# Kernel optimization log

Hardware: AMD Instinct MI355X
Metric: run time of the kernel (lower is better)

## Reference

```python
import jax, jax.numpy as jnp
import numpy as np

V = 20000
E = 40000
NODE_IN = 74
EDGE_IN = 12
D = 64            # node_out_feats
EH = 128          # edge_hidden_feats
STEPS = 6         # num_step_message_passing


def setup_inputs() -> dict:
    key = jax.random.key(0)
    ks = jax.random.split(key, 16)
    s = lambda k, shape, scale=0.05: jax.random.normal(k, shape, dtype=jnp.float32) * scale
    return {
        "node_feats": jax.random.normal(ks[0], (V, NODE_IN), dtype=jnp.float32),
        "edge_feats": jax.random.normal(ks[1], (E, EDGE_IN), dtype=jnp.float32),
        "src": jax.random.randint(ks[2], (E,), 0, V),
        "dst": jax.random.randint(ks[3], (E,), 0, V),
        # project_node_feats: Linear(NODE_IN, D) + ReLU
        "proj_W": s(ks[4], (D, NODE_IN)),
        "proj_b": jnp.zeros((D,), jnp.float32),
        # NNConv edge network: Linear(EDGE_IN, EH) -> ReLU -> Linear(EH, D*D)
        "en_W1": s(ks[5], (EH, EDGE_IN)),
        "en_b1": jnp.zeros((EH,), jnp.float32),
        "en_W2": s(ks[6], (D * D, EH)),
        "en_b2": jnp.zeros((D * D,), jnp.float32),
        # NNConv output bias
        "conv_b": jnp.zeros((D,), jnp.float32),
        # single-layer GRU (PyTorch gate order r, z, n)
        "gru_Wih": s(ks[7], (3 * D, D)),
        "gru_Whh": s(ks[8], (3 * D, D)),
        "gru_bih": jnp.zeros((3 * D,), jnp.float32),
        "gru_bhh": jnp.zeros((3 * D,), jnp.float32),
        # MLPPredictor: Linear(2*D, 1)
        "pred_W": s(ks[9], (1, 2 * D)),
        "pred_b": jnp.zeros((1,), jnp.float32),
    }


def reference(node_feats, edge_feats, src, dst, proj_W, proj_b,
              en_W1, en_b1, en_W2, en_b2, conv_b,
              gru_Wih, gru_Whh, gru_bih, gru_bhh, pred_W, pred_b):
    nV = node_feats.shape[0]
    # project node features
    h = jax.nn.relu(node_feats @ proj_W.T + proj_b)  # (V, D)
    # per-edge weight matrices from the edge network (constant across steps)
    ew = jax.nn.relu(edge_feats @ en_W1.T + en_b1) @ en_W2.T + en_b2  # (E, D*D)
    ew = ew.reshape(-1, D, D)  # (E, D, D)

    def step(h, _):
        # NNConv (aggregator='sum'): m_e = h[src_e] @ W_e, sum at dst, + bias
        m = jnp.einsum('ei,eio->eo', h[src], ew)               # (E, D)
        neigh = jax.ops.segment_sum(m, dst, num_segments=nV)   # (V, D)
        x = jax.nn.relu(neigh + conv_b)
        # GRU update; hidden == h (they coincide in the original loop)
        gi = x @ gru_Wih.T + gru_bih
        gh = h @ gru_Whh.T + gru_bhh
        i_r, i_z, i_n = jnp.split(gi, 3, axis=-1)
        h_r, h_z, h_n = jnp.split(gh, 3, axis=-1)
        r = jax.nn.sigmoid(i_r + h_r)
        z = jax.nn.sigmoid(i_z + h_z)
        n = jnp.tanh(i_n + r * h_n)
        h_new = (1.0 - z) * n + z * h
        return h_new, None

    h, _ = jax.lax.scan(step, h, None, length=STEPS)
    # MLPPredictor: per-edge gather-concat-linear
    score = jnp.concatenate([h[src], h[dst]], axis=1) @ pred_W.T + pred_b  # (E, 1)
    return score
```

## Files before the change

### kernel.cpp

```cpp
#include <hip/hip_runtime.h>
#include <hip/hip_bf16.h>
#include <cstdint>

#define NV 20000
#define NE 40000
#define NODE_IN 74
#define EDGE_IN 12
#define D 64
#define EHID 128
#define NSTEPS 6

typedef __bf16 bf16x8 __attribute__((ext_vector_type(8)));
typedef float f32x4 __attribute__((ext_vector_type(4)));

__global__ __launch_bounds__(256) void k_proj(const float* __restrict__ nf,
                                              const float* __restrict__ W,
                                              const float* __restrict__ b,
                                              float* __restrict__ h,
                                              float* __restrict__ neigh) {
  __shared__ float sn[4][NODE_IN];
  int tid = threadIdx.x;
  int nb = blockIdx.x * 4;
  for (int idx = tid; idx < 4 * NODE_IN; idx += 256) {
    int r = idx / NODE_IN, c = idx % NODE_IN;
    sn[r][c] = nf[(size_t)(nb + r) * NODE_IN + c];
  }
  __syncthreads();
  int nl = tid >> 6, o = tid & 63;
  float acc = b[o];
#pragma unroll
  for (int i = 0; i < NODE_IN; ++i) acc = fmaf(sn[nl][i], W[o * NODE_IN + i], acc);
  h[(size_t)(nb + nl) * D + o] = fmaxf(acc, 0.f);
  neigh[(size_t)(nb + nl) * D + o] = 0.f;
}

__global__ __launch_bounds__(256) void k_edge1(const float* __restrict__ ef,
                                               const float* __restrict__ W1,
                                               const float* __restrict__ b1,
                                               __hip_bfloat16* __restrict__ t_bf) {
  __shared__ float se[2][EDGE_IN];
  int tid = threadIdx.x;
  int eb = blockIdx.x * 2;
  if (tid < 2 * EDGE_IN)
    se[tid / EDGE_IN][tid % EDGE_IN] =
        ef[(size_t)(eb + tid / EDGE_IN) * EDGE_IN + tid % EDGE_IN];
  __syncthreads();
  int el = tid >> 7, k = tid & 127;
  float acc = b1[k];
#pragma unroll
  for (int j = 0; j < EDGE_IN; ++j) acc = fmaf(se[el][j], W1[k * EDGE_IN + j], acc);
  t_bf[(size_t)(eb + el) * EHID + k] = __float2bfloat16(fmaxf(acc, 0.f));
}

__global__ __launch_bounds__(256) void k_cvt_w2(const float* __restrict__ W2,
                                                __hip_bfloat16* __restrict__ w2b) {
  int idx = blockIdx.x * 256 + threadIdx.x;
  if (idx < D * D * EHID) w2b[idx] = __float2bfloat16(W2[idx]);
}

__global__ __launch_bounds__(256) void k_b2t(const float* __restrict__ b2,
                                             __hip_bfloat16* __restrict__ b2t) {
  int idx = blockIdx.x * 256 + threadIdx.x;
  int o = idx >> 6, i = idx & 63;
  b2t[o * 64 + i] = __float2bfloat16(b2[i * 64 + o]);
}

__global__ __launch_bounds__(256) void k_build_b(const float* __restrict__ Wih,
                                                 const float* __restrict__ Whh,
                                                 __hip_bfloat16* __restrict__ Bhi,
                                                 __hip_bfloat16* __restrict__ Blo) {
  int idx = blockIdx.x * 256 + threadIdx.x;
  int n = idx >> 7, k = idx & 127;
  int o = n & 63, cls = n >> 6;
  float v;
  if (cls == 0)      v = (k < 64) ? Wih[o * 64 + k]         : Whh[o * 64 + (k - 64)];
  else if (cls == 1) v = (k < 64) ? Wih[(64 + o) * 64 + k]  : Whh[(64 + o) * 64 + (k - 64)];
  else if (cls == 2) v = (k < 64) ? Wih[(128 + o) * 64 + k] : 0.f;
  else               v = (k < 64) ? 0.f                     : Whh[(128 + o) * 64 + (k - 64)];
  __hip_bfloat16 hi = __float2bfloat16(v);
  Bhi[idx] = hi;
  Blo[idx] = __float2bfloat16(v - __bfloat162float(hi));
}

__global__ __launch_bounds__(512, 2) void k_msg(const float* __restrict__ h,
                                                const __hip_bfloat16* __restrict__ t_bf,
                                                const __hip_bfloat16* __restrict__ w2,
                                                const __hip_bfloat16* __restrict__ b2t,
                                                const int* __restrict__ src,
                                                const int* __restrict__ dst,
                                                float* __restrict__ neigh) {
  __shared__ __hip_bfloat16 W2s[512 * 128];
  __shared__ __hip_bfloat16 Hs[4][32 * 64];
  int tid = threadIdx.x;
  int bx = blockIdx.x;
  int cg = bx >> 6, ih = (bx >> 5) & 1, s = bx & 31;
  int lane = tid & 63, lr = lane & 15, lq = lane >> 4;
  int wave = tid >> 6;
  int team = wave >> 1, mthalf = wave & 1;
  int lane128 = tid & 127;
  const int ocol = cg * 16 + lr;

#pragma unroll
  for (int it = 0; it < 16; ++it) {
    int chunk = it * 512 + tid;
    int row = chunk >> 4, c = chunk & 15;
    int ig = row >> 4, ol = row & 15;
    const __hip_bfloat16* gp =
        w2 + ((size_t)((ih * 32 + ig) * 64 + cg * 16 + ol)) * EHID + c * 8;
    *(bf16x8*)(W2s + row * 128 + ((c ^ ol) * 8)) = *(const bf16x8*)gp;
  }
  bf16x8 b2frag = *(const bf16x8*)(b2t + (size_t)ocol * 64 + ih * 32 + lq * 8);

  int nt = (s < 31) ? 20 : 5;

#pragma unroll 1
  for (int r5 = 0; r5 < 5; ++r5) {
    int t = r5 * 4 + team;
    int e0t = s * 1280 + t * 64;
    bool valid = (t < nt);
    __syncthreads();
    if (valid) {
      int e_l = lane128 & 63, hh = lane128 >> 6;
      int s_e = src[e0t + e_l];
      const float* hrow = h + (size_t)s_e * D + ih * 32 + hh * 16;
#pragma unroll
      for (int j4 = 0; j4 < 4; ++j4) {
        float4 hv = *(const float4*)(hrow + j4 * 4);
        int i0 = hh * 16 + j4 * 4;
        Hs[team][(i0 + 0) * 64 + e_l] = __float2bfloat16(hv.x);
        Hs[team][(i0 + 1) * 64 + e_l] = __float2bfloat16(hv.y);
        Hs[team][(i0 + 2) * 64 + e_l] = __float2bfloat16(hv.z);
        Hs[team][(i0 + 3) * 64 + e_l] = __float2bfloat16(hv.w);
      }
    }
    __syncthreads();
    if (!valid) continue;

    const __hip_bfloat16* Ht = Hs[team];
    int mt2 = mthalf * 2;
    bf16x8 tf[2][4];
#pragma unroll
    for (int mt = 0; mt < 2; ++mt)
#pragma unroll
      for (int ks = 0; ks < 4; ++ks)
        tf[mt][ks] = *(const bf16x8*)(t_bf + (size_t)(e0t + (mt2 + mt) * 16 + lr) * EHID +
                                      ks * 32 + lq * 8);
    f32x4 C0, C1;
    {
      bf16x8 af0, af1;
#pragma unroll
      for (int j = 0; j < 8; ++j) {
        af0[j] = *(const __bf16*)(Ht + (lq * 8 + j) * 64 + mt2 * 16 + lr);
        af1[j] = *(const __bf16*)(Ht + (lq * 8 + j) * 64 + (mt2 + 1) * 16 + lr);
      }
      f32x4 z = {0.f, 0.f, 0.f, 0.f};
      C0 = __builtin_amdgcn_mfma_f32_16x16x32_bf16(af0, b2frag, z, 0, 0, 0);
      C1 = __builtin_amdgcn_mfma_f32_16x16x32_bf16(af1, b2frag, z, 0, 0, 0);
    }
    int sw0 = (((0 * 4 + lq) ^ lr) * 8);
    int sw1 = (((1 * 4 + lq) ^ lr) * 8);
    int sw2 = (((2 * 4 + lq) ^ lr) * 8);
    int sw3 = (((3 * 4 + lq) ^ lr) * 8);
    int e0q0 = mt2 * 16 + lq * 4;
    int e0q1 = (mt2 + 1) * 16 + lq * 4;

#pragma unroll 2
    for (int ig = 0; ig < 32; ++ig) {
      const __hip_bfloat16* Wr = W2s + (ig * 16 + lr) * 128;
      bf16x8 f0 = *(const bf16x8*)(Wr + sw0);
      bf16x8 f1 = *(const bf16x8*)(Wr + sw1);
      bf16x8 f2 = *(const bf16x8*)(Wr + sw2);
      bf16x8 f3 = *(const bf16x8*)(Wr + sw3);
      uint2 hA = *(const uint2*)(Ht + ig * 64 + e0q0);
      uint2 hB = *(const uint2*)(Ht + ig * 64 + e0q1);
      f32x4 P0 = {0.f, 0.f, 0.f, 0.f};
      P0 = __builtin_amdgcn_mfma_f32_16x16x32_bf16(tf[0][0], f0, P0, 0, 0, 0);
      P0 = __builtin_amdgcn_mfma_f32_16x16x32_bf16(tf[0][1], f1, P0, 0, 0, 0);
      P0 = __builtin_amdgcn_mfma_f32_16x16x32_bf16(tf[0][2], f2, P0, 0, 0, 0);
      P0 = __builtin_amdgcn_mfma_f32_16x16x32_bf16(tf[0][3], f3, P0, 0, 0, 0);
      f32x4 P1 = {0.f, 0.f, 0.f, 0.f};
      P1 = __builtin_amdgcn_mfma_f32_16x16x32_bf16(tf[1][0], f0, P1, 0, 0, 0);
      P1 = __builtin_amdgcn_mfma_f32_16x16x32_bf16(tf[1][1], f1, P1, 0, 0, 0);
      P1 = __builtin_amdgcn_mfma_f32_16x16x32_bf16(tf[1][2], f2, P1, 0, 0, 0);
      P1 = __builtin_amdgcn_mfma_f32_16x16x32_bf16(tf[1][3], f3, P1, 0, 0, 0);
      C0[0] = fmaf(__uint_as_float(hA.x << 16), P0[0], C0[0]);
      C0[1] = fmaf(__uint_as_float(hA.x & 0xffff0000u), P0[1], C0[1]);
      C0[2] = fmaf(__uint_as_float(hA.y << 16), P0[2], C0[2]);
      C0[3] = fmaf(__uint_as_float(hA.y & 0xffff0000u), P0[3], C0[3]);
      C1[0] = fmaf(__uint_as_float(hB.x << 16), P1[0], C1[0]);
      C1[1] = fmaf(__uint_as_float(hB.x & 0xffff0000u), P1[1], C1[1]);
      C1[2] = fmaf(__uint_as_float(hB.y << 16), P1[2], C1[2]);
      C1[3] = fmaf(__uint_as_float(hB.y & 0xffff0000u), P1[3], C1[3]);
    }
#pragma unroll
    for (int r = 0; r < 4; ++r) {
      int ea = e0t + e0q0 + r;
      atomicAdd(neigh + (size_t)dst[ea] * D + ocol, C0[r]);
      int eb = e0t + e0q1 + r;
      atomicAdd(neigh + (size_t)dst[eb] * D + ocol, C1[r]);
    }
  }
}

__global__ __launch_bounds__(256) void k_gru(float* __restrict__ neigh,
                                             float* __restrict__ h,
                                             const __hip_bfloat16* __restrict__ Bhi,
                                             const __hip_bfloat16* __restrict__ Blo,
                                             const float* __restrict__ cb,
                                             const float* __restrict__ bih,
                                             const float* __restrict__ bhh) {
  __shared__ __hip_bfloat16 Ahi[64 * 128];
  __shared__ __hip_bfloat16 Alo[64 * 128];
  int tid = threadIdx.x;
  int n0 = blockIdx.x * 64;
  for (int idx = tid; idx < 64 * 64; idx += 256) {
    int node = idx >> 6, f = idx & 63;
    int gn = n0 + node;
    int gc = gn < NV ? gn : NV - 1;
    float xv = fmaxf(neigh[(size_t)gc * D + f] + cb[f], 0.f);
    if (gn < NV) neigh[(size_t)gn * D + f] = 0.f;
    float hv = h[(size_t)gc * D + f];
    __hip_bfloat16 xh = __float2bfloat16(xv);
    __hip_bfloat16 hh = __float2bfloat16(hv);
    Ahi[node * 128 + f] = xh;
    Ahi[node * 128 + 64 + f] = hh;
    Alo[node * 128 + f] = __float2bfloat16(xv - __bfloat162float(xh));
    Alo[node * 128 + 64 + f] = __float2bfloat16(hv - __bfloat162float(hh));
  }
  __syncthreads();
  int wave = tid >> 6, lane = tid & 63;
  int lr = lane & 15, lq = lane >> 4;
  f32x4 acc[4][4] = {};
#pragma unroll
  for (int ks = 0; ks < 4; ++ks) {
    int koff = ks * 32 + lq * 8;
    bf16x8 ah[4], al[4], bh[4], bl[4];
#pragma unroll
    for (int mt = 0; mt < 4; ++mt) {
      ah[mt] = *(const bf16x8*)(Ahi + (mt * 16 + lr) * 128 + koff);
      al[mt] = *(const bf16x8*)(Alo + (mt * 16 + lr) * 128 + koff);
    }
#pragma unroll
    for (int cls = 0; cls < 4; ++cls) {
      int n = cls * 64 + wave * 16 + lr;
      bh[cls] = *(const bf16x8*)(Bhi + (size_t)n * 128 + koff);
      bl[cls] = *(const bf16x8*)(Blo + (size_t)n * 128 + koff);
    }
#pragma unroll
    for (int mt = 0; mt < 4; ++mt)
#pragma unroll
      for (int cls = 0; cls < 4; ++cls) {
        acc[mt][cls] = __builtin_amdgcn_mfma_f32_16x16x32_bf16(ah[mt], bh[cls], acc[mt][cls], 0, 0, 0);
        acc[mt][cls] = __builtin_amdgcn_mfma_f32_16x16x32_bf16(al[mt], bh[cls], acc[mt][cls], 0, 0, 0);
        acc[mt][cls] = __builtin_amdgcn_mfma_f32_16x16x32_bf16(ah[mt], bl[cls], acc[mt][cls], 0, 0, 0);
      }
  }
  int o = wave * 16 + lr;
  float b_r = bih[o] + bhh[o];
  float b_z = bih[64 + o] + bhh[64 + o];
  float b_in = bih[128 + o];
  float b_hn = bhh[128 + o];
#pragma unroll
  for (int mt = 0; mt < 4; ++mt) {
#pragma unroll
    for (int r = 0; r < 4; ++r) {
      int gn = n0 + mt * 16 + lq * 4 + r;
      if (gn < NV) {
        float rs = acc[mt][0][r] + b_r;
        float zs = acc[mt][1][r] + b_z;
        float inn = acc[mt][2][r] + b_in;
        float hnn = acc[mt][3][r] + b_hn;
        float rg = 1.f / (1.f + __expf(-rs));
        float zg = 1.f / (1.f + __expf(-zs));
        float a = inn + rg * hnn;
        a = fminf(fmaxf(a, -15.f), 15.f);
        float e2 = __expf(2.f * a);
        float nn = (e2 - 1.f) / (e2 + 1.f);
        float hold = h[(size_t)gn * D + o];
        h[(size_t)gn * D + o] = (1.f - zg) * nn + zg * hold;
      }
    }
  }
}

__global__ __launch_bounds__(256) void k_pred(const float* __restrict__ h,
                                              const int* __restrict__ src,
                                              const int* __restrict__ dst,
                                              const float* __restrict__ pW,
                                              const float* __restrict__ pb,
                                              float* __restrict__ out) {
  int wave = threadIdx.x >> 6, lane = threadIdx.x & 63;
  int e = blockIdx.x * 4 + wave;
  int s = src[e], d2 = dst[e];
  float v = h[(size_t)s * D + lane] * pW[lane] + h[(size_t)d2 * D + lane] * pW[64 + lane];
#pragma unroll
  for (int off = 32; off >= 1; off >>= 1) v += __shfl_xor(v, off, 64);
  if (lane == 0) out[e] = v + pb[0];
}

extern "C" void kernel_launch(void* const* d_in, const int* in_sizes, int n_in,
                              void* d_out, int out_size, void* d_ws, size_t ws_size,
                              hipStream_t stream) {
  const float* node_feats = (const float*)d_in[0];
  const float* edge_feats = (const float*)d_in[1];
  const int* src = (const int*)d_in[2];
  const int* dst = (const int*)d_in[3];
  const float* proj_W = (const float*)d_in[4];
  const float* proj_b = (const float*)d_in[5];
  const float* en_W1 = (const float*)d_in[6];
  const float* en_b1 = (const float*)d_in[7];
  const float* en_W2 = (const float*)d_in[8];
  const float* en_b2 = (const float*)d_in[9];
  const float* conv_b = (const float*)d_in[10];
  const float* gru_Wih = (const float*)d_in[11];
  const float* gru_Whh = (const float*)d_in[12];
  const float* gru_bih = (const float*)d_in[13];
  const float* gru_bhh = (const float*)d_in[14];
  const float* pred_W = (const float*)d_in[15];
  const float* pred_b = (const float*)d_in[16];

  char* ws = (char*)d_ws;
  size_t off = 0;
  auto walloc = [&](size_t bytes) -> void* {
    void* p = ws + off;
    off = (off + bytes + 255) & ~(size_t)255;
    return p;
  };
  float* h = (float*)walloc((size_t)NV * D * 4);
  float* neigh = (float*)walloc((size_t)NV * D * 4);
  __hip_bfloat16* t_bf = (__hip_bfloat16*)walloc((size_t)NE * EHID * 2);
  __hip_bfloat16* w2_bf = (__hip_bfloat16*)walloc((size_t)D * D * EHID * 2);
  __hip_bfloat16* b2t = (__hip_bfloat16*)walloc((size_t)D * D * 2);
  __hip_bfloat16* Bhi = (__hip_bfloat16*)walloc((size_t)256 * 128 * 2);
  __hip_bfloat16* Blo = (__hip_bfloat16*)walloc((size_t)256 * 128 * 2);

  k_proj<<<NV / 4, 256, 0, stream>>>(node_feats, proj_W, proj_b, h, neigh);
  k_edge1<<<NE / 2, 256, 0, stream>>>(edge_feats, en_W1, en_b1, t_bf);
  k_cvt_w2<<<(D * D * EHID + 255) / 256, 256, 0, stream>>>(en_W2, w2_bf);
  k_b2t<<<(D * D + 255) / 256, 256, 0, stream>>>(en_b2, b2t);
  k_build_b<<<128, 256, 0, stream>>>(gru_Wih, gru_Whh, Bhi, Blo);
  for (int s = 0; s < NSTEPS; ++s) {
    k_msg<<<256, 512, 0, stream>>>(h, t_bf, w2_bf, b2t, src, dst, neigh);
    k_gru<<<(NV + 63) / 64, 256, 0, stream>>>(neigh, h, Bhi, Blo, conv_b, gru_bih, gru_bhh);
  }
  k_pred<<<NE / 4, 256, 0, stream>>>(h, src, dst, pred_W, pred_b, (float*)d_out);
}
```

Before: 593.6 us.

## Split msg waves over input-feature halves and shrink GRU tile to 32 nodes

In the message kernel, each wave pair now splits the 32 input-feature groups between its two waves and processes all four edge tiles, instead of splitting edge tiles. Each wave now issues twice as many atomics, and each edge's partial sums from the two waves are combined through global atomics. The GRU kernel moves from 64-node to 32-node blocks, which doubles the block count and removes the bounds checks because 20000 divides evenly by 32. The trade-off is more atomic traffic and more register pressure from tf[4][4] in exchange for better load balance and occupancy.

```diff
diff --git a/kernel.cpp b/kernel.cpp
--- a/kernel.cpp
+++ b/kernel.cpp
@@ -96,7 +96,7 @@
   int cg = bx >> 6, ih = (bx >> 5) & 1, s = bx & 31;
   int lane = tid & 63, lr = lane & 15, lq = lane >> 4;
   int wave = tid >> 6;
-  int team = wave >> 1, mthalf = wave & 1;
+  int team = wave >> 1, ihw = wave & 1;
   int lane128 = tid & 127;
   const int ocol = cg * 16 + lr;
 
@@ -137,67 +137,62 @@
     if (!valid) continue;
 
     const __hip_bfloat16* Ht = Hs[team];
-    int mt2 = mthalf * 2;
-    bf16x8 tf[2][4];
-#pragma unroll
-    for (int mt = 0; mt < 2; ++mt)
+    bf16x8 tf[4][4];
+#pragma unroll
+    for (int mt = 0; mt < 4; ++mt)
 #pragma unroll
       for (int ks = 0; ks < 4; ++ks)
-        tf[mt][ks] = *(const bf16x8*)(t_bf + (size_t)(e0t + (mt2 + mt) * 16 + lr) * EHID +
+        tf[mt][ks] = *(const bf16x8*)(t_bf + (size_t)(e0t + mt * 16 + lr) * EHID +
                                       ks * 32 + lq * 8);
-    f32x4 C0, C1;
-    {
-      bf16x8 af0, af1;
-#pragma unroll
-      for (int j = 0; j < 8; ++j) {
-        af0[j] = *(const __bf16*)(Ht + (lq * 8 + j) * 64 + mt2 * 16 + lr);
-        af1[j] = *(const __bf16*)(Ht + (lq * 8 + j) * 64 + (mt2 + 1) * 16 + lr);
-      }
-      f32x4 z = {0.f, 0.f, 0.f, 0.f};
-      C0 = __builtin_amdgcn_mfma_f32_16x16x32_bf16(af0, b2frag, z, 0, 0, 0);
-      C1 = __builtin_amdgcn_mfma_f32_16x16x32_bf16(af1, b2frag, z, 0, 0, 0);
+    f32x4 C[4];
+    if (ihw == 0) {
+#pragma unroll
+      for (int mt = 0; mt < 4; ++mt) {
+        bf16x8 af;
+#pragma unroll
+        for (int j = 0; j < 8; ++j)
+          af[j] = *(const __bf16*)(Ht + (lq * 8 + j) * 64 + mt * 16 + lr);
+        f32x4 z = {0.f, 0.f, 0.f, 0.f};
+        C[mt] = __builtin_amdgcn_mfma_f32_16x16x32_bf16(af, b2frag, z, 0, 0, 0);
+      }
+    } else {
+#pragma unroll
+      for (int mt = 0; mt < 4; ++mt) C[mt] = f32x4{0.f, 0.f, 0.f, 0.f};
     }
     int sw0 = (((0 * 4 + lq) ^ lr) * 8);
     int sw1 = (((1 * 4 + lq) ^ lr) * 8);
     int sw2 = (((2 * 4 + lq) ^ lr) * 8);
     int sw3 = (((3 * 4 + lq) ^ lr) * 8);
-    int e0q0 = mt2 * 16 + lq * 4;
-    int e0q1 = (mt2 + 1) * 16 + lq * 4;
 
 #pragma unroll 2
-    for (int ig = 0; ig < 32; ++ig) {
+    for (int igl = 0; igl < 16; ++igl) {
+      int ig = ihw * 16 + igl;
       const __hip_bfloat16* Wr = W2s + (ig * 16 + lr) * 128;
       bf16x8 f0 = *(const bf16x8*)(Wr + sw0);
       bf16x8 f1 = *(const bf16x8*)(Wr + sw1);
       bf16x8 f2 = *(const bf16x8*)(Wr + sw2);
       bf16x8 f3 = *(const bf16x8*)(Wr + sw3);
-      uint2 hA = *(const uint2*)(Ht + ig * 64 + e0q0);
-      uint2 hB = *(const uint2*)(Ht + ig * 64 + e0q1);
-      f32x4 P0 = {0.f, 0.f, 0.f, 0.f};
-      P0 = __builtin_amdgcn_mfma_f32_16x16x32_bf16(tf[0][0], f0, P0, 0, 0, 0);
-      P0 = __builtin_amdgcn_mfma_f32_16x16x32_bf16(tf[0][1], f1, P0, 0, 0, 0);
-      P0 = __builtin_amdgcn_mfma_f32_16x16x32_bf16(tf[0][2], f2, P0, 0, 0, 0);
-      P0 = __builtin_amdgcn_mfma_f32_16x16x32_bf16(tf[0][3], f3, P0, 0, 0, 0);
-      f32x4 P1 = {0.f, 0.f, 0.f, 0.f};
-      P1 = __builtin_amdgcn_mfma_f32_16x16x32_bf16(tf[1][0], f0, P1, 0, 0, 0);
-      P1 = __builtin_amdgcn_mfma_f32_16x16x32_bf16(tf[1][1], f1, P1, 0, 0, 0);
-      P1 = __builtin_amdgcn_mfma_f32_16x16x32_bf16(tf[1][2], f2, P1, 0, 0, 0);
-      P1 = __builtin_amdgcn_mfma_f32_16x16x32_bf16(tf[1][3], f3, P1, 0, 0, 0);
-      C0[0] = fmaf(__uint_as_float(hA.x << 16), P0[0], C0[0]);
-      C0[1] = fmaf(__uint_as_float(hA.x & 0xffff0000u), P0[1], C0[1]);
-      C0[2] = fmaf(__uint_as_float(hA.y << 16), P0[2], C0[2]);
-      C0[3] = fmaf(__uint_as_float(hA.y & 0xffff0000u), P0[3], C0[3]);
-      C1[0] = fmaf(__uint_as_float(hB.x << 16), P1[0], C1[0]);
-      C1[1] = fmaf(__uint_as_float(hB.x & 0xffff0000u), P1[1], C1[1]);
-      C1[2] = fmaf(__uint_as_float(hB.y << 16), P1[2], C1[2]);
-      C1[3] = fmaf(__uint_as_float(hB.y & 0xffff0000u), P1[3], C1[3]);
-    }
-#pragma unroll
-    for (int r = 0; r < 4; ++r) {
-      int ea = e0t + e0q0 + r;
-      atomicAdd(neigh + (size_t)dst[ea] * D + ocol, C0[r]);
-      int eb = e0t + e0q1 + r;
-      atomicAdd(neigh + (size_t)dst[eb] * D + ocol, C1[r]);
+#pragma unroll
+      for (int mt = 0; mt < 4; ++mt) {
+        f32x4 P = {0.f, 0.f, 0.f, 0.f};
+        P = __builtin_amdgcn_mfma_f32_16x16x32_bf16(tf[mt][0], f0, P, 0, 0, 0);
+        P = __builtin_amdgcn_mfma_f32_16x16x32_bf16(tf[mt][1], f1, P, 0, 0, 0);
+        P = __builtin_amdgcn_mfma_f32_16x16x32_bf16(tf[mt][2], f2, P, 0, 0, 0);
+        P = __builtin_amdgcn_mfma_f32_16x16x32_bf16(tf[mt][3], f3, P, 0, 0, 0);
+        uint2 hA = *(const uint2*)(Ht + ig * 64 + mt * 16 + lq * 4);
+        C[mt][0] = fmaf(__uint_as_float(hA.x << 16), P[0], C[mt][0]);
+        C[mt][1] = fmaf(__uint_as_float(hA.x & 0xffff0000u), P[1], C[mt][1]);
+        C[mt][2] = fmaf(__uint_as_float(hA.y << 16), P[2], C[mt][2]);
+        C[mt][3] = fmaf(__uint_as_float(hA.y & 0xffff0000u), P[3], C[mt][3]);
+      }
+    }
+#pragma unroll
+    for (int mt = 0; mt < 4; ++mt) {
+#pragma unroll
+      for (int r = 0; r < 4; ++r) {
+        int ea = e0t + mt * 16 + lq * 4 + r;
+        atomicAdd(neigh + (size_t)dst[ea] * D + ocol, C[mt][r]);
+      }
     }
   }
 }
@@ -209,17 +204,16 @@
                                              const float* __restrict__ cb,
                                              const float* __restrict__ bih,
                                              const float* __restrict__ bhh) {
-  __shared__ __hip_bfloat16 Ahi[64 * 128];
-  __shared__ __hip_bfloat16 Alo[64 * 128];
+  __shared__ __hip_bfloat16 Ahi[32 * 128];
+  __shared__ __hip_bfloat16 Alo[32 * 128];
   int tid = threadIdx.x;
-  int n0 = blockIdx.x * 64;
-  for (int idx = tid; idx < 64 * 64; idx += 256) {
+  int n0 = blockIdx.x * 32;
+  for (int idx = tid; idx < 32 * 64; idx += 256) {
     int node = idx >> 6, f = idx & 63;
     int gn = n0 + node;
-    int gc = gn < NV ? gn : NV - 1;
-    float xv = fmaxf(neigh[(size_t)gc * D + f] + cb[f], 0.f);
-    if (gn < NV) neigh[(size_t)gn * D + f] = 0.f;
-    float hv = h[(size_t)gc * D + f];
+    float xv = fmaxf(neigh[(size_t)gn * D + f] + cb[f], 0.f);
+    neigh[(size_t)gn * D + f] = 0.f;
+    float hv = h[(size_t)gn * D + f];
     __hip_bfloat16 xh = __float2bfloat16(xv);
     __hip_bfloat16 hh = __float2bfloat16(hv);
     Ahi[node * 128 + f] = xh;
@@ -230,13 +224,13 @@
   __syncthreads();
   int wave = tid >> 6, lane = tid & 63;
   int lr = lane & 15, lq = lane >> 4;
-  f32x4 acc[4][4] = {};
+  f32x4 acc[2][4] = {};
 #pragma unroll
   for (int ks = 0; ks < 4; ++ks) {
     int koff = ks * 32 + lq * 8;
-    bf16x8 ah[4], al[4], bh[4], bl[4];
-#pragma unroll
-    for (int mt = 0; mt < 4; ++mt) {
+    bf16x8 ah[2], al[2], bh[4], bl[4];
+#pragma unroll
+    for (int mt = 0; mt < 2; ++mt) {
       ah[mt] = *(const bf16x8*)(Ahi + (mt * 16 + lr) * 128 + koff);
       al[mt] = *(const bf16x8*)(Alo + (mt * 16 + lr) * 128 + koff);
     }
@@ -247,7 +241,7 @@
       bl[cls] = *(const bf16x8*)(Blo + (size_t)n * 128 + koff);
     }
 #pragma unroll
-    for (int mt = 0; mt < 4; ++mt)
+    for (int mt = 0; mt < 2; ++mt)
 #pragma unroll
       for (int cls = 0; cls < 4; ++cls) {
         acc[mt][cls] = __builtin_amdgcn_mfma_f32_16x16x32_bf16(ah[mt], bh[cls], acc[mt][cls], 0, 0, 0);
@@ -261,24 +255,22 @@
   float b_in = bih[128 + o];
   float b_hn = bhh[128 + o];
 #pragma unroll
-  for (int mt = 0; mt < 4; ++mt) {
+  for (int mt = 0; mt < 2; ++mt) {
 #pragma unroll
     for (int r = 0; r < 4; ++r) {
       int gn = n0 + mt * 16 + lq * 4 + r;
-      if (gn < NV) {
-        float rs = acc[mt][0][r] + b_r;
-        float zs = acc[mt][1][r] + b_z;
-        float inn = acc[mt][2][r] + b_in;
-        float hnn = acc[mt][3][r] + b_hn;
-        float rg = 1.f / (1.f + __expf(-rs));
-        float zg = 1.f / (1.f + __expf(-zs));
-        float a = inn + rg * hnn;
-        a = fminf(fmaxf(a, -15.f), 15.f);
-        float e2 = __expf(2.f * a);
-        float nn = (e2 - 1.f) / (e2 + 1.f);
-        float hold = h[(size_t)gn * D + o];
-        h[(size_t)gn * D + o] = (1.f - zg) * nn + zg * hold;
-      }
+      float rs = acc[mt][0][r] + b_r;
+      float zs = acc[mt][1][r] + b_z;
+      float inn = acc[mt][2][r] + b_in;
+      float hnn = acc[mt][3][r] + b_hn;
+      float rg = 1.f / (1.f + __expf(-rs));
+      float zg = 1.f / (1.f + __expf(-zs));
+      float a = inn + rg * hnn;
+      a = fminf(fmaxf(a, -15.f), 15.f);
+      float e2 = __expf(2.f * a);
+      float nn = (e2 - 1.f) / (e2 + 1.f);
+      float hold = h[(size_t)gn * D + o];
+      h[(size_t)gn * D + o] = (1.f - zg) * nn + zg * hold;
     }
   }
 }
@@ -341,7 +333,7 @@
   k_build_b<<<128, 256, 0, stream>>>(gru_Wih, gru_Whh, Bhi, Blo);
   for (int s = 0; s < NSTEPS; ++s) {
     k_msg<<<256, 512, 0, stream>>>(h, t_bf, w2_bf, b2t, src, dst, neigh);
-    k_gru<<<(NV + 63) / 64, 256, 0, stream>>>(neigh, h, Bhi, Blo, conv_b, gru_bih, gru_bhh);
+    k_gru<<<NV / 32, 256, 0, stream>>>(neigh, h, Bhi, Blo, conv_b, gru_bih, gru_bhh);
   }
   k_pred<<<NE / 4, 256, 0, stream>>>(h, src, dst, pred_W, pred_b, (float*)d_out);
 }
```

Result: slower. 691.7 us (+16.5%).
